# Performance work log

Hardware: AMD Instinct MI355X
Metric: run time of the kernel (lower is better)

## Reference

```python
import jax, jax.numpy as jnp
import numpy as np

V = 32000      # vocab
D = 192        # d_model
NL = 8         # n_layers
DS = 64        # d_state (ssm_dim)
EXP = 2
K = 3          # conv kernel
NC = 2         # num_classes
DI = EXP * D   # d_inner = 384
DTR = (D + 15) // 16  # dt_rank = 12
EPS = 1e-6


def setup_inputs() -> dict:
    key = jax.random.key(0)
    ks = jax.random.split(key, 10)
    n = lambda k, shape, s=0.02: (jax.random.normal(k, shape) * s).astype(jnp.float32)
    input_ids = jax.random.randint(ks[0], (4, 512), 0, V, dtype=jnp.int32)
    embed = n(ks[1], (V, D))
    cls = jax.random.normal(ks[2], (1, 1, D), jnp.float32)
    norm_ws = jnp.ones((NL, D), jnp.float32)
    in_proj_ws = n(ks[3], (NL, 2 * DI, D))
    conv_ws = n(ks[4], (NL, DI, K), 0.1)
    conv_bs = jnp.zeros((NL, DI), jnp.float32)
    x_proj_ws = n(ks[5], (NL, DTR + 2 * DS, DI))
    dt_proj_ws = n(ks[6], (NL, DI, DTR), 0.1)
    dt_proj_bs = jnp.full((NL, DI), jnp.log(jnp.expm1(0.01)), jnp.float32)  # softplus^-1(0.01)
    A_logs = jnp.tile(jnp.log(jnp.arange(1, DS + 1, dtype=jnp.float32))[None, None, :], (NL, DI, 1))
    Ds = jnp.ones((NL, DI), jnp.float32)
    out_proj_ws = n(ks[7], (NL, D, DI))
    final_norm_w = jnp.ones((D,), jnp.float32)
    head_w = embed[:NC]  # tied embeddings
    head_b = jnp.zeros((NC,), jnp.float32)
    return dict(input_ids=input_ids, cls=cls, embed=embed, norm_ws=norm_ws,
                in_proj_ws=in_proj_ws, conv_ws=conv_ws, conv_bs=conv_bs,
                x_proj_ws=x_proj_ws, dt_proj_ws=dt_proj_ws, dt_proj_bs=dt_proj_bs,
                A_logs=A_logs, Ds=Ds, out_proj_ws=out_proj_ws,
                final_norm_w=final_norm_w, head_w=head_w, head_b=head_b)


def rmsnorm(x, w):
    return w * x * jax.lax.rsqrt(jnp.mean(x * x, axis=-1, keepdims=True) + EPS)


def ssm_scan(dA, dBu, C):
    # dA, dBu: [B,L,DI,DS]; C: [B,L,DS] -> y: [B,L,DI]
    dA_t = jnp.moveaxis(dA, 1, 0)
    dBu_t = jnp.moveaxis(dBu, 1, 0)
    C_t = jnp.moveaxis(C, 1, 0)
    h0 = jnp.zeros(dA.shape[:1] + dA.shape[2:], dA.dtype)  # [B,DI,DS]
    def step(h, inp):
        a, bu, c = inp
        h = a * h + bu
        return h, jnp.einsum('bds,bs->bd', h, c)
    _, ys = jax.lax.scan(step, h0, (dA_t, dBu_t, C_t))
    return jnp.moveaxis(ys, 0, 1)


def mamba_layer(x, p):
    nw, ipw, cw, cb, xpw, dpw, dpb, Al, Dp, opw = p
    xn = rmsnorm(x, nw)
    xz = jnp.einsum('bld,ed->ble', xn, ipw)        # [B,L,2*DI]
    u0, z = jnp.split(xz, 2, axis=-1)
    # causal depthwise conv along time
    lhs = jnp.swapaxes(u0, 1, 2)                   # [B,DI,L]
    rhs = cw[:, None, :]                           # [DI,1,K]
    conv = jax.lax.conv_general_dilated(lhs, rhs, (1,), [(K - 1, 0)],
                                        dimension_numbers=('NCH', 'OIH', 'NCH'),
                                        feature_group_count=DI)
    u = jax.nn.silu(jnp.swapaxes(conv, 1, 2) + cb) # [B,L,DI]
    xdbl = jnp.einsum('bld,ed->ble', u, xpw)
    dt, Bm, Cm = jnp.split(xdbl, [DTR, DTR + DS], axis=-1)
    delta = jax.nn.softplus(jnp.einsum('blr,dr->bld', dt, dpw) + dpb)  # [B,L,DI]
    A = -jnp.exp(Al)                               # [DI,DS]
    dA = jnp.exp(delta[..., None] * A)             # [B,L,DI,DS]
    dBu = delta[..., None] * Bm[:, :, None, :] * u[..., None]
    y = ssm_scan(dA, dBu, Cm)
    y = (y + u * Dp) * jax.nn.silu(z)
    return jnp.einsum('bld,ed->ble', y, opw)


def reference(input_ids, cls, embed, norm_ws, in_proj_ws, conv_ws, conv_bs,
              x_proj_ws, dt_proj_ws, dt_proj_bs, A_logs, Ds, out_proj_ws,
              final_norm_w, head_w, head_b):
    x = embed[input_ids]                           # [B,L,D]
    B = x.shape[0]
    x = jnp.concatenate([x, jnp.broadcast_to(cls, (B, 1, D))], axis=1)
    params = (norm_ws, in_proj_ws, conv_ws, conv_bs, x_proj_ws,
              dt_proj_ws, dt_proj_bs, A_logs, Ds, out_proj_ws)
    def layer_step(h, p):
        return h + mamba_layer(h, p), None
    x, _ = jax.lax.scan(layer_step, x, params)
    x = rmsnorm(x, final_norm_w)
    return x[:, -1] @ head_w.T + head_b
```

## Files before the change

### kernel.cpp

```cpp
#include <hip/hip_runtime.h>
#include <math.h>

#define D 192
#define NL 8
#define DS_ 64
#define DI 384
#define DTR 12
#define LSEQ 513
#define BATCH 4
#define M_ROWS (BATCH*LSEQ)
#define XD 140
#define EPS 1e-6f
#define CH 64
#define CL 9

typedef __attribute__((ext_vector_type(8))) short bf16x8;
typedef __attribute__((ext_vector_type(4))) float f32x4;

__device__ __forceinline__ float sigmoidf_(float x){ return 1.0f/(1.0f+__expf(-x)); }
__device__ __forceinline__ unsigned bfpack(float a, float b){
  unsigned ua = __float_as_uint(a); ua += 0x7FFFu + ((ua>>16)&1u);
  unsigned ub = __float_as_uint(b); ub += 0x7FFFu + ((ub>>16)&1u);
  return (ua>>16) | (ub & 0xFFFF0000u);
}
__device__ __forceinline__ float bf2f(unsigned short u){ return __uint_as_float(((unsigned)u)<<16); }
__device__ __forceinline__ unsigned short f2bf(float f){
  unsigned u=__float_as_uint(f); u += 0x7FFFu + ((u>>16)&1u); return (unsigned short)(u>>16);
}

__global__ void k_cvt(const float* __restrict__ src, unsigned short* __restrict__ dst, int n4){
  int i = blockIdx.x*256 + threadIdx.x;
  if (i >= n4) return;
  float4 v = *(const float4*)(src + (size_t)i*4);
  uint2 p; p.x = bfpack(v.x,v.y); p.y = bfpack(v.z,v.w);
  *(uint2*)(dst + (size_t)i*4) = p;
}

__global__ void k_embed(const int* __restrict__ ids, const float* __restrict__ embed,
                        const float* __restrict__ cls, float* __restrict__ x){
  int row = blockIdx.x;
  int b = row / LSEQ, l = row % LSEQ;
  int d = threadIdx.x;
  float v;
  if (l < LSEQ-1) v = embed[(long)ids[b*(LSEQ-1)+l]*D + d];
  else            v = cls[d];
  x[row*D + d] = v;
}

__global__ __launch_bounds__(256) void k_norm(const float* __restrict__ x, const float* __restrict__ nw,
                                              unsigned short* __restrict__ xn){
  int row = blockIdx.x*4 + (threadIdx.x>>6);
  int lane = threadIdx.x & 63;
  if (row >= M_ROWS) return;
  const float* xr = x + (size_t)row*D;
  float v0 = xr[lane], v1 = xr[lane+64], v2 = xr[lane+128];
  float ss = v0*v0 + v1*v1 + v2*v2;
  #pragma unroll
  for (int off = 32; off > 0; off >>= 1) ss += __shfl_xor(ss, off, 64);
  float sc = rsqrtf(ss*(1.0f/D) + EPS);
  xn[(size_t)row*D + lane      ] = f2bf(v0*sc*nw[lane]);
  xn[(size_t)row*D + lane + 64 ] = f2bf(v1*sc*nw[lane+64]);
  xn[(size_t)row*D + lane + 128] = f2bf(v2*sc*nw[lane+128]);
}

template<int ACC, int K, int N>
__global__ __launch_bounds__(256) void k_mfma(
    const unsigned short* __restrict__ A, const unsigned short* __restrict__ W,
    float* __restrict__ out)
{
  __shared__ __align__(16) unsigned short LA[64*200];
  __shared__ __align__(16) unsigned short LB[64*200];
  const int t = threadIdx.x;
  const int w = t >> 6, l = t & 63;
  const int row0 = blockIdx.x*64, col0 = blockIdx.y*64;
  const int lo = l & 15, hi = l >> 4;

  f32x4 acc[4] = {};

  for (int kc = 0; kc < K; kc += 192) {
    __syncthreads();
    #pragma unroll
    for (int it = 0; it < 6; ++it) {
      int i = t + it*256;
      int r = i / 24, c16 = i % 24;
      int rg = row0 + r;
      uint4 v = {0,0,0,0};
      if (rg < M_ROWS) v = *(const uint4*)(A + (size_t)rg*K + kc + c16*8);
      *(uint4*)(&LA[r*200 + c16*8]) = v;
    }
    #pragma unroll
    for (int it = 0; it < 6; ++it) {
      int i = t + it*256;
      int r = i / 24, c16 = i % 24;
      int cg = col0 + r;
      uint4 v = {0,0,0,0};
      if (N % 64 == 0 || cg < N) {
        if (cg < N) v = *(const uint4*)(W + (size_t)cg*K + kc + c16*8);
      }
      *(uint4*)(&LB[r*200 + c16*8]) = v;
    }
    __syncthreads();
    #pragma unroll
    for (int ks = 0; ks < 6; ++ks) {
      bf16x8 af = *(const bf16x8*)(&LA[(w*16 + lo)*200 + ks*32 + hi*8]);
      #pragma unroll
      for (int nt = 0; nt < 4; ++nt) {
        bf16x8 bfr = *(const bf16x8*)(&LB[(nt*16 + lo)*200 + ks*32 + hi*8]);
        acc[nt] = __builtin_amdgcn_mfma_f32_16x16x32_bf16(af, bfr, acc[nt], 0, 0, 0);
      }
    }
  }

  #pragma unroll
  for (int nt = 0; nt < 4; ++nt) {
    #pragma unroll
    for (int r = 0; r < 4; ++r) {
      int row = row0 + w*16 + hi*4 + r;
      int col = col0 + nt*16 + lo;
      if (row < M_ROWS && (N % 64 == 0 || col < N)) {
        if (ACC) out[(size_t)row*N + col] += acc[nt][r];
        else     out[(size_t)row*N + col]  = acc[nt][r];
      }
    }
  }
}

__global__ void k_conv(const float* __restrict__ xz, const float* __restrict__ cw,
                       const float* __restrict__ cb, float* __restrict__ u,
                       unsigned short* __restrict__ ubf){
  int idx = blockIdx.x*256 + threadIdx.x;
  if (idx >= M_ROWS*DI) return;
  int row = idx / DI, c = idx % DI;
  int l = row % LSEQ;
  float w0 = cw[c*3+0], w1 = cw[c*3+1], w2 = cw[c*3+2];
  float s = cb[c];
  float x0 = (l >= 2) ? xz[(row-2)*(2*DI) + c] : 0.f;
  float x1 = (l >= 1) ? xz[(row-1)*(2*DI) + c] : 0.f;
  float x2 = xz[row*(2*DI) + c];
  s += x0*w0 + x1*w1 + x2*w2;
  s = s * sigmoidf_(s);
  u[idx] = s;
  ubf[idx] = f2bf(s);
}

template<int COMPY>
__global__ __launch_bounds__(64) void k_scanA(
    const float* __restrict__ u, const float* __restrict__ xdbl,
    const float* __restrict__ dpw, const float* __restrict__ dpb,
    unsigned short* __restrict__ hend, float* __restrict__ Ssum,
    const float* __restrict__ xz, const float* __restrict__ Dp,
    unsigned short* __restrict__ g)
{
  int blk = blockIdx.x;
  int c  = blk % CH;
  int t1 = blk / CH;
  int dg = t1 % 6;
  int b  = t1 / 6;
  int lane = threadIdx.x;
  int d  = dg*64 + lane;
  int l0 = c*CL;
  int nr = LSEQ - l0; if (nr > CL) nr = CL;

  long hoff = ((long)(b*CH + c)*DS_)*DI + d;

  if (nr <= 0) {
    if (!COMPY) {
      #pragma unroll
      for (int s = 0; s < DS_; ++s) hend[hoff + (long)s*DI] = 0;
      Ssum[(b*CH + c)*DI + d] = 0.f;
    }
    return;
  }

  __shared__ __align__(16) float xs[CL*XD];

  {
    const float4* src = (const float4*)(xdbl + (size_t)(b*LSEQ + l0)*XD);
    float4* dst = (float4*)xs;
    float4 tmp[5];
    #pragma unroll
    for (int i = 0; i < 5; ++i) {
      int idx = lane + i*64;
      if (idx < (CL*XD)/4) tmp[i] = src[idx];
    }
    #pragma unroll
    for (int i = 0; i < 5; ++i) {
      int idx = lane + i*64;
      if (idx < (CL*XD)/4) dst[idx] = tmp[i];
    }
  }

  float dw[12];
  {
    const float4* p = (const float4*)(dpw + (size_t)d*DTR);
    float4 q0=p[0], q1=p[1], q2=p[2];
    dw[0]=q0.x;dw[1]=q0.y;dw[2]=q0.z;dw[3]=q0.w;
    dw[4]=q1.x;dw[5]=q1.y;dw[6]=q1.z;dw[7]=q1.w;
    dw[8]=q2.x;dw[9]=q2.y;dw[10]=q2.z;dw[11]=q2.w;
  }
  float db = dpb[d];
  float Dpd = COMPY ? Dp[d] : 0.f;

  float h[DS_];
  if (COMPY) {
    #pragma unroll
    for (int s = 0; s < DS_; ++s) h[s] = bf2f(hend[hoff + (long)s*DI]);
  } else {
    #pragma unroll
    for (int s = 0; s < DS_; ++s) h[s] = 0.f;
  }

  __syncthreads();

  const float* ubase = u + (size_t)(b*LSEQ + l0)*DI + d;
  const float* zbase = xz + (size_t)(b*LSEQ + l0)*(2*DI) + DI + d;
  unsigned short* gbase = g + (size_t)(b*LSEQ + l0)*DI + d;
  float u_cur = ubase[0];
  float S = 0.f;
  const float* xr = xs;

  for (int r = 0; r < nr; ++r) {
    float u_nxt = (r+1 < nr) ? ubase[(size_t)(r+1)*DI] : 0.f;
    float4 t0 = *(const float4*)(xr+0);
    float4 t1v = *(const float4*)(xr+4);
    float4 t2 = *(const float4*)(xr+8);
    float p0 = db + t0.x*dw[0] + t0.y*dw[1] + t0.z*dw[2] + t0.w*dw[3];
    float p1 = t1v.x*dw[4] + t1v.y*dw[5] + t1v.z*dw[6] + t1v.w*dw[7];
    float p2 = t2.x*dw[8] + t2.y*dw[9] + t2.z*dw[10] + t2.w*dw[11];
    float dlt = p0 + p1 + p2;
    dlt = fmaxf(dlt, 0.f) + log1pf(__expf(-fabsf(dlt)));

    float r1 = __expf(-dlt);
    float r2 = r1*r1, r3 = r2*r1, r4 = r2*r2;
    float c0 = dlt * u_cur;
    float b4 = 1.f;
    float yv0=0.f, yv1=0.f, yv2=0.f, yv3=0.f;
    #pragma unroll
    for (int gi = 0; gi < 16; ++gi) {
      float e0 = b4*r1, e1 = b4*r2, e2 = b4*r3, e3 = b4*r4;
      float4 Bv = *(const float4*)(xr + DTR + 4*gi);
      h[4*gi+0] = e0*h[4*gi+0] + c0*Bv.x;
      h[4*gi+1] = e1*h[4*gi+1] + c0*Bv.y;
      h[4*gi+2] = e2*h[4*gi+2] + c0*Bv.z;
      h[4*gi+3] = e3*h[4*gi+3] + c0*Bv.w;
      if (COMPY) {
        float4 Cv = *(const float4*)(xr + DTR + DS_ + 4*gi);
        yv0 += h[4*gi+0]*Cv.x;
        yv1 += h[4*gi+1]*Cv.y;
        yv2 += h[4*gi+2]*Cv.z;
        yv3 += h[4*gi+3]*Cv.w;
      }
      b4 *= r4;
    }
    if (COMPY) {
      float yv = (yv0+yv1)+(yv2+yv3);
      float zv = zbase[(size_t)r*(2*DI)];
      float gv = (yv + u_cur*Dpd) * (zv * sigmoidf_(zv));
      gbase[(size_t)r*DI] = f2bf(gv);
    } else {
      S += dlt;
    }
    u_cur = u_nxt;
    xr += XD;
  }

  if (!COMPY) {
    #pragma unroll
    for (int s = 0; s < DS_; ++s) hend[hoff + (long)s*DI] = f2bf(h[s]);
    Ssum[(b*CH + c)*DI + d] = S;
  }
}

__global__ __launch_bounds__(256) void k_scan2(unsigned short* __restrict__ hend,
                                               const float* __restrict__ Ssum){
  int idx = blockIdx.x*256 + threadIdx.x;
  int d = idx % DI;
  int t = idx / DI;
  int s = t % DS_;
  int b = t / DS_;
  float ns1 = -(float)(s+1);
  float h = 0.f;
  for (int c = 0; c < CH; ++c) {
    long off = ((long)(b*CH + c)*DS_ + s)*DI + d;
    float he = bf2f(hend[off]);
    float a  = __expf(ns1 * Ssum[(b*CH + c)*DI + d]);
    hend[off] = f2bf(h);
    h = a*h + he;
  }
}

__global__ __launch_bounds__(64) void k_head(const float* __restrict__ x, const float* __restrict__ fnw,
      const float* __restrict__ hw, const float* __restrict__ hb, float* __restrict__ out){
  int b = blockIdx.x;
  int s = threadIdx.x;
  const float* xr = x + (long)(b*LSEQ + LSEQ-1)*D;
  float xv[3];
  float ss = 0.f;
  #pragma unroll
  for (int j = 0; j < 3; ++j) { float v = xr[s + 64*j]; xv[j] = v; ss += v*v; }
  #pragma unroll
  for (int off = 32; off > 0; off >>= 1) ss += __shfl_xor(ss, off, 64);
  float sc = rsqrtf(ss*(1.0f/D) + EPS);
  #pragma unroll
  for (int j = 0; j < 3; ++j) xv[j] = xv[j]*sc*fnw[s+64*j];
  for (int c = 0; c < 2; ++c) {
    float p = 0.f;
    #pragma unroll
    for (int j = 0; j < 3; ++j) p += xv[j]*hw[c*D + s + 64*j];
    #pragma unroll
    for (int off = 32; off > 0; off >>= 1) p += __shfl_xor(p, off, 64);
    if (s == 0) out[b*2 + c] = p + hb[c];
  }
}

extern "C" void kernel_launch(void* const* d_in, const int* in_sizes, int n_in,
                              void* d_out, int out_size, void* d_ws, size_t ws_size,
                              hipStream_t stream) {
  const int*   ids        = (const int*)  d_in[0];
  const float* cls        = (const float*)d_in[1];
  const float* embed      = (const float*)d_in[2];
  const float* norm_ws    = (const float*)d_in[3];
  const float* in_proj_ws = (const float*)d_in[4];
  const float* conv_ws    = (const float*)d_in[5];
  const float* conv_bs    = (const float*)d_in[6];
  const float* x_proj_ws  = (const float*)d_in[7];
  const float* dt_proj_ws = (const float*)d_in[8];
  const float* dt_proj_bs = (const float*)d_in[9];
  const float* Ds         = (const float*)d_in[11];
  const float* out_proj_ws= (const float*)d_in[12];
  const float* final_norm_w=(const float*)d_in[13];
  const float* head_w     = (const float*)d_in[14];
  const float* head_b     = (const float*)d_in[15];
  float* out = (float*)d_out;

  char* p = (char*)d_ws;
  float* x     = (float*)p;            p += (size_t)M_ROWS*D*4;
  float* xz    = (float*)p;            p += (size_t)M_ROWS*2*DI*4;
  float* u     = (float*)p;            p += (size_t)M_ROWS*DI*4;
  float* xdbl  = (float*)p;            p += (size_t)M_ROWS*XD*4;
  unsigned short* xn  = (unsigned short*)p; p += (size_t)M_ROWS*D*2;
  unsigned short* ubf = (unsigned short*)p; p += (size_t)M_ROWS*DI*2;
  unsigned short* g   = (unsigned short*)p; p += (size_t)M_ROWS*DI*2;
  unsigned short* hend= (unsigned short*)p; p += (size_t)BATCH*CH*DS_*DI*2;
  float* Ssum  = (float*)p;            p += (size_t)BATCH*CH*DI*4;
  unsigned short* wip = (unsigned short*)p; p += (size_t)NL*2*DI*D*2;
  unsigned short* wxp = (unsigned short*)p; p += (size_t)NL*XD*DI*2;
  unsigned short* wop = (unsigned short*)p; p += (size_t)NL*D*DI*2;

  k_cvt<<<(NL*2*DI*D/4 + 255)/256, 256, 0, stream>>>(in_proj_ws, wip, NL*2*DI*D/4);
  k_cvt<<<(NL*XD*DI/4 + 255)/256, 256, 0, stream>>>(x_proj_ws, wxp, NL*XD*DI/4);
  k_cvt<<<(NL*D*DI/4 + 255)/256, 256, 0, stream>>>(out_proj_ws, wop, NL*D*DI/4);

  k_embed<<<M_ROWS, D, 0, stream>>>(ids, embed, cls, x);
  for (int il = 0; il < NL; ++il) {
    const float* nw  = norm_ws     + il*D;
    const float* cw  = conv_ws     + il*DI*3;
    const float* cb  = conv_bs     + il*DI;
    const float* dpw = dt_proj_ws  + il*DI*DTR;
    const float* dpb = dt_proj_bs  + il*DI;
    const float* Dp  = Ds          + il*DI;
    const unsigned short* ipw = wip + (size_t)il*2*DI*D;
    const unsigned short* xpw = wxp + (size_t)il*XD*DI;
    const unsigned short* opw = wop + (size_t)il*D*DI;

    k_norm<<<(M_ROWS+3)/4, 256, 0, stream>>>(x, nw, xn);
    dim3 g0(33, 12);
    k_mfma<0,192,768><<<g0,256,0,stream>>>(xn, ipw, xz);
    k_conv<<<(M_ROWS*DI+255)/256,256,0,stream>>>(xz, cw, cb, u, ubf);
    dim3 g1(33, 3);
    k_mfma<0,384,140><<<g1,256,0,stream>>>(ubf, xpw, xdbl);
    k_scanA<0><<<BATCH*6*CH, 64, 0, stream>>>(u, xdbl, dpw, dpb, hend, Ssum, xz, Dp, g);
    k_scan2<<<BATCH*DS_*DI/256, 256, 0, stream>>>(hend, Ssum);
    k_scanA<1><<<BATCH*6*CH, 64, 0, stream>>>(u, xdbl, dpw, dpb, hend, Ssum, xz, Dp, g);
    dim3 g2(33, 3);
    k_mfma<1,384,192><<<g2,256,0,stream>>>(g, opw, x);
  }
  k_head<<<BATCH, 64, 0, stream>>>(x, final_norm_w, head_w, head_b, out);
}
```

Measured before the change: 747.2 us.

## Fuse RMSNorm into in_proj GEMM and recompute conv+SiLU in consumers

RMSNorm is folded into the in_proj GEMM prologue, which also moves to 128-wide N tiles. The depthwise conv and SiLU are no longer run as a separate kernel: the x_proj GEMM and both scan passes recompute u from xz on the fly. This removes two kernel launches per layer and the u, ubf and xn intermediate buffers. In exchange the conv arithmetic runs three times and the GEMM loaders do more global reads.

```diff
diff --git a/kernel.cpp b/kernel.cpp
--- a/kernel.cpp
+++ b/kernel.cpp
@@ -47,20 +47,161 @@
   x[row*D + d] = v;
 }
 
-__global__ __launch_bounds__(256) void k_norm(const float* __restrict__ x, const float* __restrict__ nw,
-                                              unsigned short* __restrict__ xn){
-  int row = blockIdx.x*4 + (threadIdx.x>>6);
-  int lane = threadIdx.x & 63;
-  if (row >= M_ROWS) return;
-  const float* xr = x + (size_t)row*D;
-  float v0 = xr[lane], v1 = xr[lane+64], v2 = xr[lane+128];
-  float ss = v0*v0 + v1*v1 + v2*v2;
-  #pragma unroll
-  for (int off = 32; off > 0; off >>= 1) ss += __shfl_xor(ss, off, 64);
-  float sc = rsqrtf(ss*(1.0f/D) + EPS);
-  xn[(size_t)row*D + lane      ] = f2bf(v0*sc*nw[lane]);
-  xn[(size_t)row*D + lane + 64 ] = f2bf(v1*sc*nw[lane+64]);
-  xn[(size_t)row*D + lane + 128] = f2bf(v2*sc*nw[lane+128]);
+__global__ __launch_bounds__(256) void k_in(
+    const float* __restrict__ x, const float* __restrict__ nw,
+    const unsigned short* __restrict__ W, float* __restrict__ out)
+{
+  __shared__ __align__(16) unsigned short LA[64*200];
+  __shared__ __align__(16) unsigned short LB[128*104];
+  __shared__ float scale_s[64];
+
+  const int t = threadIdx.x;
+  const int w = t >> 6, l = t & 63;
+  const int lo = l & 15, hi = l >> 4;
+  const int row0 = blockIdx.x*64, col0 = blockIdx.y*128;
+
+  {
+    int r = t >> 2, j = t & 3;
+    float ss = 0.f;
+    int rg = row0 + r;
+    if (rg < M_ROWS) {
+      const float* xr = x + (size_t)rg*D;
+      #pragma unroll
+      for (int c4 = 0; c4 < 12; ++c4) {
+        float4 v = *(const float4*)(xr + (j + c4*4)*4);
+        ss += v.x*v.x + v.y*v.y + v.z*v.z + v.w*v.w;
+      }
+    }
+    ss += __shfl_xor(ss, 1, 64);
+    ss += __shfl_xor(ss, 2, 64);
+    if (j == 0) scale_s[r] = rsqrtf(ss*(1.0f/D) + EPS);
+  }
+  __syncthreads();
+
+  #pragma unroll
+  for (int it = 0; it < 12; ++it) {
+    int i = t + it*256;
+    int r = i / 48, c4 = i % 48;
+    int k = c4*4;
+    int rg = row0 + r;
+    float4 v = {0.f,0.f,0.f,0.f};
+    if (rg < M_ROWS) {
+      v = *(const float4*)(x + (size_t)rg*D + k);
+      float4 nwv = *(const float4*)(nw + k);
+      float sc = scale_s[r];
+      v.x *= sc*nwv.x; v.y *= sc*nwv.y; v.z *= sc*nwv.z; v.w *= sc*nwv.w;
+    }
+    uint2 p; p.x = bfpack(v.x,v.y); p.y = bfpack(v.z,v.w);
+    *(uint2*)(&LA[r*200 + k]) = p;
+  }
+
+  f32x4 acc[8] = {};
+  #pragma unroll
+  for (int kb = 0; kb < 2; ++kb) {
+    __syncthreads();
+    #pragma unroll
+    for (int it = 0; it < 6; ++it) {
+      int i = t + it*256;
+      int r = i / 12, c8 = i % 12;
+      int k = c8*8;
+      int cg = col0 + r;
+      uint4 v = *(const uint4*)(W + (size_t)cg*D + kb*96 + k);
+      *(uint4*)(&LB[r*104 + k]) = v;
+    }
+    __syncthreads();
+    #pragma unroll
+    for (int ks = 0; ks < 3; ++ks) {
+      bf16x8 af = *(const bf16x8*)(&LA[(w*16 + lo)*200 + kb*96 + ks*32 + hi*8]);
+      #pragma unroll
+      for (int nf = 0; nf < 8; ++nf) {
+        bf16x8 bfr = *(const bf16x8*)(&LB[(nf*16 + lo)*104 + ks*32 + hi*8]);
+        acc[nf] = __builtin_amdgcn_mfma_f32_16x16x32_bf16(af, bfr, acc[nf], 0, 0, 0);
+      }
+    }
+  }
+  #pragma unroll
+  for (int nf = 0; nf < 8; ++nf) {
+    #pragma unroll
+    for (int r = 0; r < 4; ++r) {
+      int row = row0 + w*16 + hi*4 + r;
+      int col = col0 + nf*16 + lo;
+      if (row < M_ROWS) out[(size_t)row*(2*DI) + col] = acc[nf][r];
+    }
+  }
+}
+
+__global__ __launch_bounds__(256) void k_xp(
+    const float* __restrict__ xz, const float* __restrict__ cw, const float* __restrict__ cb,
+    const unsigned short* __restrict__ W, float* __restrict__ out)
+{
+  __shared__ __align__(16) unsigned short LA[64*200];
+  __shared__ __align__(16) unsigned short LB[64*200];
+  const int t = threadIdx.x;
+  const int w = t >> 6, l = t & 63;
+  const int lo = l & 15, hi = l >> 4;
+  const int row0 = blockIdx.x*64, col0 = blockIdx.y*64;
+
+  f32x4 acc[4] = {};
+
+  for (int kc = 0; kc < DI; kc += 192) {
+    __syncthreads();
+    #pragma unroll
+    for (int it = 0; it < 12; ++it) {
+      int i = t + it*256;
+      int r = i / 48, c4 = i % 48;
+      int ch = kc + c4*4;
+      int rg = row0 + r;
+      float4 uv = {0.f,0.f,0.f,0.f};
+      if (rg < M_ROWS) {
+        int ll = rg % LSEQ;
+        const float* base = xz + (size_t)rg*(2*DI) + ch;
+        float4 a2 = *(const float4*)(base);
+        float4 a1 = (ll>=1) ? *(const float4*)(base - 2*DI) : (float4){0,0,0,0};
+        float4 a0 = (ll>=2) ? *(const float4*)(base - 4*DI) : (float4){0,0,0,0};
+        const float* cwp = cw + (size_t)ch*3;
+        float4 q0 = *(const float4*)(cwp);
+        float4 q1 = *(const float4*)(cwp+4);
+        float4 q2 = *(const float4*)(cwp+8);
+        float4 cbv = *(const float4*)(cb + ch);
+        float s0 = cbv.x + a0.x*q0.x + a1.x*q0.y + a2.x*q0.z;
+        float s1 = cbv.y + a0.y*q0.w + a1.y*q1.x + a2.y*q1.y;
+        float s2 = cbv.z + a0.z*q1.z + a1.z*q1.w + a2.z*q2.x;
+        float s3 = cbv.w + a0.w*q2.y + a1.w*q2.z + a2.w*q2.w;
+        uv.x = s0*sigmoidf_(s0); uv.y = s1*sigmoidf_(s1);
+        uv.z = s2*sigmoidf_(s2); uv.w = s3*sigmoidf_(s3);
+      }
+      uint2 p; p.x = bfpack(uv.x,uv.y); p.y = bfpack(uv.z,uv.w);
+      *(uint2*)(&LA[r*200 + c4*4]) = p;
+    }
+    #pragma unroll
+    for (int it = 0; it < 6; ++it) {
+      int i = t + it*256;
+      int r = i / 24, c16 = i % 24;
+      int cg = col0 + r;
+      uint4 v = {0,0,0,0};
+      if (cg < XD) v = *(const uint4*)(W + (size_t)cg*DI + kc + c16*8);
+      *(uint4*)(&LB[r*200 + c16*8]) = v;
+    }
+    __syncthreads();
+    #pragma unroll
+    for (int ks = 0; ks < 6; ++ks) {
+      bf16x8 af = *(const bf16x8*)(&LA[(w*16 + lo)*200 + ks*32 + hi*8]);
+      #pragma unroll
+      for (int nt = 0; nt < 4; ++nt) {
+        bf16x8 bfr = *(const bf16x8*)(&LB[(nt*16 + lo)*200 + ks*32 + hi*8]);
+        acc[nt] = __builtin_amdgcn_mfma_f32_16x16x32_bf16(af, bfr, acc[nt], 0, 0, 0);
+      }
+    }
+  }
+  #pragma unroll
+  for (int nt = 0; nt < 4; ++nt) {
+    #pragma unroll
+    for (int r = 0; r < 4; ++r) {
+      int row = row0 + w*16 + hi*4 + r;
+      int col = col0 + nt*16 + lo;
+      if (row < M_ROWS && col < XD) out[(size_t)row*XD + col] = acc[nt][r];
+    }
+  }
 }
 
 template<int ACC, int K, int N>
@@ -76,7 +217,6 @@
   const int lo = l & 15, hi = l >> 4;
 
   f32x4 acc[4] = {};
-
   for (int kc = 0; kc < K; kc += 192) {
     __syncthreads();
     #pragma unroll
@@ -110,7 +250,6 @@
       }
     }
   }
-
   #pragma unroll
   for (int nt = 0; nt < 4; ++nt) {
     #pragma unroll
@@ -125,30 +264,13 @@
   }
 }
 
-__global__ void k_conv(const float* __restrict__ xz, const float* __restrict__ cw,
-                       const float* __restrict__ cb, float* __restrict__ u,
-                       unsigned short* __restrict__ ubf){
-  int idx = blockIdx.x*256 + threadIdx.x;
-  if (idx >= M_ROWS*DI) return;
-  int row = idx / DI, c = idx % DI;
-  int l = row % LSEQ;
-  float w0 = cw[c*3+0], w1 = cw[c*3+1], w2 = cw[c*3+2];
-  float s = cb[c];
-  float x0 = (l >= 2) ? xz[(row-2)*(2*DI) + c] : 0.f;
-  float x1 = (l >= 1) ? xz[(row-1)*(2*DI) + c] : 0.f;
-  float x2 = xz[row*(2*DI) + c];
-  s += x0*w0 + x1*w1 + x2*w2;
-  s = s * sigmoidf_(s);
-  u[idx] = s;
-  ubf[idx] = f2bf(s);
-}
-
 template<int COMPY>
 __global__ __launch_bounds__(64) void k_scanA(
-    const float* __restrict__ u, const float* __restrict__ xdbl,
+    const float* __restrict__ xz, const float* __restrict__ xdbl,
     const float* __restrict__ dpw, const float* __restrict__ dpb,
+    const float* __restrict__ cw, const float* __restrict__ cb,
+    const float* __restrict__ Dp,
     unsigned short* __restrict__ hend, float* __restrict__ Ssum,
-    const float* __restrict__ xz, const float* __restrict__ Dp,
     unsigned short* __restrict__ g)
 {
   int blk = blockIdx.x;
@@ -173,7 +295,6 @@
   }
 
   __shared__ __align__(16) float xs[CL*XD];
-
   {
     const float4* src = (const float4*)(xdbl + (size_t)(b*LSEQ + l0)*XD);
     float4* dst = (float4*)xs;
@@ -199,6 +320,7 @@
     dw[8]=q2.x;dw[9]=q2.y;dw[10]=q2.z;dw[11]=q2.w;
   }
   float db = dpb[d];
+  float cw0 = cw[d*3], cw1 = cw[d*3+1], cw2 = cw[d*3+2], cbd = cb[d];
   float Dpd = COMPY ? Dp[d] : 0.f;
 
   float h[DS_];
@@ -212,15 +334,20 @@
 
   __syncthreads();
 
-  const float* ubase = u + (size_t)(b*LSEQ + l0)*DI + d;
-  const float* zbase = xz + (size_t)(b*LSEQ + l0)*(2*DI) + DI + d;
+  const float* zrow = xz + (size_t)(b*LSEQ + l0)*(2*DI) + d;
   unsigned short* gbase = g + (size_t)(b*LSEQ + l0)*DI + d;
-  float u_cur = ubase[0];
   float S = 0.f;
   const float* xr = xs;
 
   for (int r = 0; r < nr; ++r) {
-    float u_nxt = (r+1 < nr) ? ubase[(size_t)(r+1)*DI] : 0.f;
+    int ll = l0 + r;
+    const float* base = zrow + (size_t)r*(2*DI);
+    float a2 = base[0];
+    float a1 = (ll>=1) ? base[-(2*DI)]   : 0.f;
+    float a0 = (ll>=2) ? base[-(4*DI)]   : 0.f;
+    float uu = cbd + a0*cw0 + a1*cw1 + a2*cw2;
+    uu = uu * sigmoidf_(uu);
+
     float4 t0 = *(const float4*)(xr+0);
     float4 t1v = *(const float4*)(xr+4);
     float4 t2 = *(const float4*)(xr+8);
@@ -232,7 +359,7 @@
 
     float r1 = __expf(-dlt);
     float r2 = r1*r1, r3 = r2*r1, r4 = r2*r2;
-    float c0 = dlt * u_cur;
+    float c0 = dlt * uu;
     float b4 = 1.f;
     float yv0=0.f, yv1=0.f, yv2=0.f, yv3=0.f;
     #pragma unroll
@@ -254,13 +381,12 @@
     }
     if (COMPY) {
       float yv = (yv0+yv1)+(yv2+yv3);
-      float zv = zbase[(size_t)r*(2*DI)];
-      float gv = (yv + u_cur*Dpd) * (zv * sigmoidf_(zv));
+      float zv = base[DI];
+      float gv = (yv + uu*Dpd) * (zv * sigmoidf_(zv));
       gbase[(size_t)r*DI] = f2bf(gv);
     } else {
       S += dlt;
     }
-    u_cur = u_nxt;
     xr += XD;
   }
 
@@ -280,6 +406,7 @@
   int b = t / DS_;
   float ns1 = -(float)(s+1);
   float h = 0.f;
+  #pragma unroll 4
   for (int c = 0; c < CH; ++c) {
     long off = ((long)(b*CH + c)*DS_ + s)*DI + d;
     float he = bf2f(hend[off]);
@@ -336,10 +463,7 @@
   char* p = (char*)d_ws;
   float* x     = (float*)p;            p += (size_t)M_ROWS*D*4;
   float* xz    = (float*)p;            p += (size_t)M_ROWS*2*DI*4;
-  float* u     = (float*)p;            p += (size_t)M_ROWS*DI*4;
   float* xdbl  = (float*)p;            p += (size_t)M_ROWS*XD*4;
-  unsigned short* xn  = (unsigned short*)p; p += (size_t)M_ROWS*D*2;
-  unsigned short* ubf = (unsigned short*)p; p += (size_t)M_ROWS*DI*2;
   unsigned short* g   = (unsigned short*)p; p += (size_t)M_ROWS*DI*2;
   unsigned short* hend= (unsigned short*)p; p += (size_t)BATCH*CH*DS_*DI*2;
   float* Ssum  = (float*)p;            p += (size_t)BATCH*CH*DI*4;
@@ -363,15 +487,13 @@
     const unsigned short* xpw = wxp + (size_t)il*XD*DI;
     const unsigned short* opw = wop + (size_t)il*D*DI;
 
-    k_norm<<<(M_ROWS+3)/4, 256, 0, stream>>>(x, nw, xn);
-    dim3 g0(33, 12);
-    k_mfma<0,192,768><<<g0,256,0,stream>>>(xn, ipw, xz);
-    k_conv<<<(M_ROWS*DI+255)/256,256,0,stream>>>(xz, cw, cb, u, ubf);
+    dim3 g0(33, 6);
+    k_in<<<g0,256,0,stream>>>(x, nw, ipw, xz);
     dim3 g1(33, 3);
-    k_mfma<0,384,140><<<g1,256,0,stream>>>(ubf, xpw, xdbl);
-    k_scanA<0><<<BATCH*6*CH, 64, 0, stream>>>(u, xdbl, dpw, dpb, hend, Ssum, xz, Dp, g);
+    k_xp<<<g1,256,0,stream>>>(xz, cw, cb, xpw, xdbl);
+    k_scanA<0><<<BATCH*6*CH, 64, 0, stream>>>(xz, xdbl, dpw, dpb, cw, cb, Dp, hend, Ssum, g);
     k_scan2<<<BATCH*DS_*DI/256, 256, 0, stream>>>(hend, Ssum);
-    k_scanA<1><<<BATCH*6*CH, 64, 0, stream>>>(u, xdbl, dpw, dpb, hend, Ssum, xz, Dp, g);
+    k_scanA<1><<<BATCH*6*CH, 64, 0, stream>>>(xz, xdbl, dpw, dpb, cw, cb, Dp, hend, Ssum, g);
     dim3 g2(33, 3);
     k_mfma<1,384,192><<<g2,256,0,stream>>>(g, opw, x);
   }
```

Result: slower. 848.7 us (+13.6%).
